# Kernel optimization log

Hardware: AMD Instinct MI355X
Metric: run time of the kernel (lower is better)

Reference implementation:

```python
import jax, jax.numpy as jnp
import numpy as np

BIT = 8          # mantissa bits (incl. sign) shared-exponent BFP
GROUP_SIZE = 16  # elements sharing one exponent


def bfp_quant(x, bit=BIT, group_size=GROUP_SIZE):
    """Block floating-point quantization: flatten, group, share max exponent per group."""
    orig_shape = x.shape
    flat = x.reshape(-1)
    n = flat.shape[0]
    pad = (-n) % group_size
    flat = jnp.pad(flat, (0, pad))
    g = flat.reshape(-1, group_size)                      # [G, group_size]
    m = jnp.max(jnp.abs(g), axis=1, keepdims=True)        # shared magnitude per group
    e = jnp.floor(jnp.log2(jnp.where(m > 0, m, 1.0)))     # shared exponent
    scale = jnp.exp2(e - (bit - 1))                       # quantization step
    qmax = 2.0 ** (bit - 1) - 1
    q = jnp.clip(jnp.round(g / scale), -qmax, qmax) * scale
    q = jnp.where(m > 0, q, 0.0)                          # all-zero groups stay zero
    return q.reshape(-1)[:n].reshape(orig_shape)


def conv2d(x, w, stride=1, padding=1):
    return jax.lax.conv_general_dilated(
        x, w,
        window_strides=(stride, stride),
        padding=((padding, padding), (padding, padding)),
        dimension_numbers=("NCHW", "OIHW", "NCHW"),
    )


def setup_inputs() -> dict:
    key = jax.random.key(0)
    k1, k2 = jax.random.split(key)
    x = jax.random.normal(k1, (64, 128, 56, 56), dtype=jnp.float32)
    fan_in = 128 * 3 * 3
    bound = 1.0 / np.sqrt(fan_in)  # kaiming_uniform_(a=sqrt(5)) -> U(-1/sqrt(fan_in), 1/sqrt(fan_in))
    w = jax.random.uniform(k2, (128, 128, 3, 3), dtype=jnp.float32,
                           minval=-bound, maxval=bound)
    return {"x": x, "w": w}


def reference(x, w):
    # BFConv2dFunction.forward: quantize both operands then conv2d (bias=None, stride=1, padding=1)
    return conv2d(bfp_quant(x), bfp_quant(w), stride=1, padding=1)
```

## Files before the change

kernel.cpp:

```cpp
#include <hip/hip_runtime.h>
#include <hip/hip_bf16.h>


using short8 = __attribute__((ext_vector_type(8))) short;
using f32x4  = __attribute__((ext_vector_type(4))) float;
using int4v  = __attribute__((ext_vector_type(4))) int;

#define XS_STRIDE_S 40
#define XS_ENT      348
#define XS_BUF_S    (XS_ENT * XS_STRIDE_S)

__device__ __forceinline__ unsigned short f2bf(float f) {
    union { float f; unsigned u; } v; v.f = f;
    return (unsigned short)(v.u >> 16);
}

__device__ __forceinline__ void quant16(const float* v, float* o) {
    float m = 0.f;
    #pragma unroll
    for (int i = 0; i < 16; ++i) m = fmaxf(m, fabsf(v[i]));
    if (m > 0.f) {
        float e     = floorf(log2f(m));
        float scale = exp2f(e - 7.0f);
        float inv   = exp2f(7.0f - e);
        #pragma unroll
        for (int i = 0; i < 16; ++i) {
            float q = rintf(v[i] * inv);
            q = fminf(fmaxf(q, -127.f), 127.f);
            o[i] = q * scale;
        }
    } else {
        #pragma unroll
        for (int i = 0; i < 16; ++i) o[i] = 0.f;
    }
}

__global__ __launch_bounds__(256) void quant_x_kernel(const float* __restrict__ x,
                                                      unsigned short* __restrict__ xq) {
    const int bid = blockIdx.x;
    const int n  = bid / 98;
    const int pb = bid % 98;
    const int t  = threadIdx.x;
    const int c  = t & 127;
    const int g  = t >> 7;
    const int p0 = pb * 32 + g * 16;

    const float* src = x + ((size_t)(n * 128 + c) * 3136 + p0);
    float v[16];
    #pragma unroll
    for (int i = 0; i < 4; ++i) {
        float4 f = *reinterpret_cast<const float4*>(src + i * 4);
        v[i*4+0] = f.x; v[i*4+1] = f.y; v[i*4+2] = f.z; v[i*4+3] = f.w;
    }
    float o[16];
    quant16(v, o);
    unsigned short* dst = xq + ((size_t)(n * 3136 + p0) * 128 + c);
    #pragma unroll
    for (int j = 0; j < 16; ++j) dst[(size_t)j * 128] = f2bf(o[j]);
}

__global__ __launch_bounds__(256) void quant_w_kernel(const float* __restrict__ w,
                                                      unsigned short* __restrict__ wq) {
    const int G = blockIdx.x * 256 + threadIdx.x;
    const int k    = G / 72;
    const int base = (G % 72) * 16;
    const float* src = w + (size_t)k * 1152 + base;
    float v[16];
    #pragma unroll
    for (int i = 0; i < 4; ++i) {
        float4 f = *reinterpret_cast<const float4*>(src + i * 4);
        v[i*4+0] = f.x; v[i*4+1] = f.y; v[i*4+2] = f.z; v[i*4+3] = f.w;
    }
    float o[16];
    quant16(v, o);
    #pragma unroll
    for (int j = 0; j < 16; ++j) {
        int idx2 = base + j;
        int c  = idx2 / 9;
        int rs = idx2 % 9;
        wq[(((size_t)(c >> 5) * 9 + rs) * 128 + k) * 32 + (c & 31)] = f2bf(o[j]);
    }
}

__global__ __launch_bounds__(256, 2) void conv_kernel(const unsigned short* __restrict__ xq,
                                                      const unsigned short* __restrict__ wq,
                                                      float* __restrict__ out) {
    __shared__ __align__(16) unsigned short Xs[2 * XS_BUF_S];

    const int bid  = blockIdx.x;
    const int n    = bid / 14;
    const int h0   = (bid % 14) * 4;
    const int t    = threadIdx.x;
    const int lane = t & 63;
    const int wave = t >> 6;
    const int mw   = wave >> 1;
    const int nw   = wave & 1;

    const unsigned short* sbase[6];
    int  soff[6];
    bool svalid[6], sact[6];
    #pragma unroll
    for (int it = 0; it < 6; ++it) {
        int i   = t + it * 256;
        bool act = i < 1392;
        int e   = i >> 2, cc = i & 3;
        int row = e / 58, pw = e % 58;
        int h   = h0 - 1 + row, w_ = pw - 1;
        bool inb = act && (unsigned)h < 56u && (unsigned)w_ < 56u;
        int gidx = inb ? (n * 3136 + h * 56 + w_) : 0;
        sbase[it]  = xq + (size_t)gidx * 128 + cc * 8;
        soff[it]   = e * XS_STRIDE_S + cc * 8;
        svalid[it] = inb;
        sact[it]   = act;
    }
    int4v sreg[6];

#define STAGE_LOAD(CB) do {                                                    \
    _Pragma("unroll")                                                          \
    for (int it = 0; it < 6; ++it)                                             \
        sreg[it] = svalid[it]                                                  \
            ? *reinterpret_cast<const int4v*>(sbase[it] + (CB) * 32)           \
            : int4v{0, 0, 0, 0};                                               \
} while (0)

#define STAGE_WRITE(BUFS) do {                                                 \
    _Pragma("unroll")                                                          \
    for (int it = 0; it < 6; ++it)                                             \
        if (sact[it])                                                          \
            *reinterpret_cast<int4v*>(Xs + (BUFS) + soff[it]) = sreg[it];      \
} while (0)

    int boff[7];
    #pragma unroll
    for (int fi = 0; fi < 7; ++fi) {
        int m  = mw * 112 + fi * 16 + (lane & 15);
        int dh = m / 56, w_ = m % 56;
        boff[fi] = (dh * 58 + w_) * XS_STRIDE_S + ((lane >> 4) * 8);
    }
    const unsigned short* wk = wq + (size_t)(nw * 64 + (lane & 15)) * 32 + ((lane >> 4) * 8);

    f32x4 acc[7][4];
    #pragma unroll
    for (int fi = 0; fi < 7; ++fi)
        #pragma unroll
        for (int ni = 0; ni < 4; ++ni)
            acc[fi][ni] = f32x4{0.f, 0.f, 0.f, 0.f};

#define RS_STEP(RS) do {                                                       \
    const int rsS = (((RS) / 3) * 58 + ((RS) % 3)) * XS_STRIDE_S;              \
    short8 a[4], b[7];                                                         \
    _Pragma("unroll")                                                          \
    for (int ni = 0; ni < 4; ++ni)                                             \
        a[ni] = *reinterpret_cast<const short8*>(wcb + (RS) * 4096 + ni * 512);\
    _Pragma("unroll")                                                          \
    for (int fi = 0; fi < 7; ++fi)                                             \
        b[fi] = *reinterpret_cast<const short8*>(Xs + bufS + boff[fi] + rsS);  \
    _Pragma("unroll")                                                          \
    for (int fi = 0; fi < 7; ++fi)                                             \
        _Pragma("unroll")                                                      \
        for (int ni = 0; ni < 4; ++ni)                                         \
            acc[fi][ni] = __builtin_amdgcn_mfma_f32_16x16x32_bf16(             \
                a[ni], b[fi], acc[fi][ni], 0, 0, 0);                           \
} while (0)

    STAGE_LOAD(0);
    STAGE_WRITE(0);
    __syncthreads();

    for (int cblk = 0; cblk < 4; ++cblk) {
        const int bufS = (cblk & 1) * XS_BUF_S;
        const unsigned short* wcb = wk + (size_t)cblk * 9 * 4096;
        RS_STEP(0);
        if (cblk < 3) STAGE_LOAD(cblk + 1);
        RS_STEP(1); RS_STEP(2); RS_STEP(3); RS_STEP(4);
        RS_STEP(5); RS_STEP(6); RS_STEP(7); RS_STEP(8);
        if (cblk < 3) STAGE_WRITE(((cblk + 1) & 1) * XS_BUF_S);
        __syncthreads();
    }

    const int pix0  = h0 * 56 + mw * 112 + (lane & 15);
    const int krow0 = n * 128 + nw * 64 + ((lane >> 4) * 4);
    #pragma unroll
    for (int fi = 0; fi < 7; ++fi)
        #pragma unroll
        for (int ni = 0; ni < 4; ++ni)
            #pragma unroll
            for (int j = 0; j < 4; ++j)
                out[(size_t)(krow0 + ni * 16 + j) * 3136 + pix0 + fi * 16] = acc[fi][ni][j];
#undef RS_STEP
#undef STAGE_LOAD
#undef STAGE_WRITE
}

extern "C" void kernel_launch(void* const* d_in, const int* in_sizes, int n_in,
                              void* d_out, int out_size, void* d_ws, size_t ws_size,
                              hipStream_t stream) {
    const float* x = (const float*)d_in[0];
    const float* w = (const float*)d_in[1];
    float* out = (float*)d_out;

    unsigned short* xq = (unsigned short*)d_ws;
    unsigned short* wq = xq + (size_t)25690112;

    quant_x_kernel<<<64 * 98, 256, 0, stream>>>(x, xq);
    quant_w_kernel<<<36,      256, 0, stream>>>(w, wq);
    conv_kernel  <<<896,      256, 0, stream>>>(xq, wq, out);
}
```

Measured before the change: 272.9 us.

## Merge quant kernels with LDS transpose, swizzle conv blocks, prefetch weight fragments

Folds the x and w quantization into one launch, and stages each 128-channel by 64-pixel tile of x through shared memory so global reads are coalesced before the per-channel group quantization. The conv kernel remaps block indices so consecutive blocks come from different images, and it fully unrolls the 36 channel-block/tap steps with a one-step-ahead register prefetch of the weight fragments. This aims to cut launch overhead and uncoalesced-access cost and to hide global weight-load latency behind the MFMAs. In exchange it uses more registers, which could hurt occupancy under the two-blocks-per-CU bound.

```diff
diff --git a/kernel.cpp b/kernel.cpp
--- a/kernel.cpp
+++ b/kernel.cpp
@@ -35,50 +35,64 @@
     }
 }
 
-__global__ __launch_bounds__(256) void quant_x_kernel(const float* __restrict__ x,
-                                                      unsigned short* __restrict__ xq) {
+__global__ __launch_bounds__(256) void quant_kernel(const float* __restrict__ x,
+                                                    const float* __restrict__ w,
+                                                    unsigned short* __restrict__ xq,
+                                                    unsigned short* __restrict__ wq) {
+    __shared__ float T[128 * 68];
     const int bid = blockIdx.x;
-    const int n  = bid / 98;
-    const int pb = bid % 98;
-    const int t  = threadIdx.x;
-    const int c  = t & 127;
-    const int g  = t >> 7;
-    const int p0 = pb * 32 + g * 16;
-
-    const float* src = x + ((size_t)(n * 128 + c) * 3136 + p0);
-    float v[16];
-    #pragma unroll
-    for (int i = 0; i < 4; ++i) {
-        float4 f = *reinterpret_cast<const float4*>(src + i * 4);
-        v[i*4+0] = f.x; v[i*4+1] = f.y; v[i*4+2] = f.z; v[i*4+3] = f.w;
-    }
-    float o[16];
-    quant16(v, o);
-    unsigned short* dst = xq + ((size_t)(n * 3136 + p0) * 128 + c);
-    #pragma unroll
-    for (int j = 0; j < 16; ++j) dst[(size_t)j * 128] = f2bf(o[j]);
-}
-
-__global__ __launch_bounds__(256) void quant_w_kernel(const float* __restrict__ w,
-                                                      unsigned short* __restrict__ wq) {
-    const int G = blockIdx.x * 256 + threadIdx.x;
-    const int k    = G / 72;
-    const int base = (G % 72) * 16;
-    const float* src = w + (size_t)k * 1152 + base;
-    float v[16];
-    #pragma unroll
-    for (int i = 0; i < 4; ++i) {
-        float4 f = *reinterpret_cast<const float4*>(src + i * 4);
-        v[i*4+0] = f.x; v[i*4+1] = f.y; v[i*4+2] = f.z; v[i*4+3] = f.w;
-    }
-    float o[16];
-    quant16(v, o);
-    #pragma unroll
-    for (int j = 0; j < 16; ++j) {
-        int idx2 = base + j;
-        int c  = idx2 / 9;
-        int rs = idx2 % 9;
-        wq[(((size_t)(c >> 5) * 9 + rs) * 128 + k) * 32 + (c & 31)] = f2bf(o[j]);
+    const int t   = threadIdx.x;
+
+    if (bid < 3136) {
+        const int n  = bid / 49;
+        const int p0 = (bid % 49) * 64;
+        const float* src = x + (size_t)n * 128 * 3136 + p0;
+
+        #pragma unroll
+        for (int i = 0; i < 8; ++i) {
+            const int c  = (t >> 4) + i * 16;
+            const int ch = t & 15;
+            *reinterpret_cast<float4*>(&T[c * 68 + ch * 4]) =
+                *reinterpret_cast<const float4*>(src + (size_t)c * 3136 + ch * 4);
+        }
+        __syncthreads();
+
+        const int c = t & 127;
+        #pragma unroll
+        for (int i = 0; i < 2; ++i) {
+            const int grp = (t >> 7) + 2 * i;
+            float v[16];
+            #pragma unroll
+            for (int j2 = 0; j2 < 4; ++j2) {
+                float4 f = *reinterpret_cast<const float4*>(&T[c * 68 + grp * 16 + j2 * 4]);
+                v[j2*4+0] = f.x; v[j2*4+1] = f.y; v[j2*4+2] = f.z; v[j2*4+3] = f.w;
+            }
+            float o[16];
+            quant16(v, o);
+            unsigned short* dst = xq + ((size_t)(n * 3136 + p0 + grp * 16)) * 128 + c;
+            #pragma unroll
+            for (int j = 0; j < 16; ++j) dst[(size_t)j * 128] = f2bf(o[j]);
+        }
+    } else {
+        const int G    = (bid - 3136) * 256 + t;
+        const int k    = G / 72;
+        const int base = (G % 72) * 16;
+        const float* src = w + (size_t)k * 1152 + base;
+        float v[16];
+        #pragma unroll
+        for (int i = 0; i < 4; ++i) {
+            float4 f = *reinterpret_cast<const float4*>(src + i * 4);
+            v[i*4+0] = f.x; v[i*4+1] = f.y; v[i*4+2] = f.z; v[i*4+3] = f.w;
+        }
+        float o[16];
+        quant16(v, o);
+        #pragma unroll
+        for (int j = 0; j < 16; ++j) {
+            int idx2 = base + j;
+            int c  = idx2 / 9;
+            int rs = idx2 % 9;
+            wq[(((size_t)(c >> 5) * 9 + rs) * 128 + k) * 32 + (c & 31)] = f2bf(o[j]);
+        }
     }
 }
 
@@ -87,7 +101,8 @@
                                                       float* __restrict__ out) {
     __shared__ __align__(16) unsigned short Xs[2 * XS_BUF_S];
 
-    const int bid  = blockIdx.x;
+    const int b0   = blockIdx.x;
+    const int bid  = (b0 & 7) * 112 + (b0 >> 3);
     const int n    = bid / 14;
     const int h0   = (bid % 14) * 4;
     const int t    = threadIdx.x;
@@ -139,6 +154,13 @@
     }
     const unsigned short* wk = wq + (size_t)(nw * 64 + (lane & 15)) * 32 + ((lane >> 4) * 8);
 
+#define LOADA(DST, STEP) do {                                                  \
+    _Pragma("unroll")                                                          \
+    for (int ni = 0; ni < 4; ++ni)                                             \
+        DST[ni] = *reinterpret_cast<const short8*>(                            \
+            wk + (size_t)(STEP) * 4096 + ni * 512);                            \
+} while (0)
+
     f32x4 acc[7][4];
     #pragma unroll
     for (int fi = 0; fi < 7; ++fi)
@@ -146,36 +168,41 @@
         for (int ni = 0; ni < 4; ++ni)
             acc[fi][ni] = f32x4{0.f, 0.f, 0.f, 0.f};
 
-#define RS_STEP(RS) do {                                                       \
-    const int rsS = (((RS) / 3) * 58 + ((RS) % 3)) * XS_STRIDE_S;              \
-    short8 a[4], b[7];                                                         \
-    _Pragma("unroll")                                                          \
-    for (int ni = 0; ni < 4; ++ni)                                             \
-        a[ni] = *reinterpret_cast<const short8*>(wcb + (RS) * 4096 + ni * 512);\
-    _Pragma("unroll")                                                          \
-    for (int fi = 0; fi < 7; ++fi)                                             \
-        b[fi] = *reinterpret_cast<const short8*>(Xs + bufS + boff[fi] + rsS);  \
-    _Pragma("unroll")                                                          \
-    for (int fi = 0; fi < 7; ++fi)                                             \
-        _Pragma("unroll")                                                      \
-        for (int ni = 0; ni < 4; ++ni)                                         \
-            acc[fi][ni] = __builtin_amdgcn_mfma_f32_16x16x32_bf16(             \
-                a[ni], b[fi], acc[fi][ni], 0, 0, 0);                           \
-} while (0)
+    short8 a_cur[4], a_nxt[4];
 
     STAGE_LOAD(0);
+    LOADA(a_cur, 0);
     STAGE_WRITE(0);
     __syncthreads();
 
-    for (int cblk = 0; cblk < 4; ++cblk) {
+    #pragma unroll
+    for (int step = 0; step < 36; ++step) {
+        const int cblk = step / 9;
+        const int rs   = step % 9;
         const int bufS = (cblk & 1) * XS_BUF_S;
-        const unsigned short* wcb = wk + (size_t)cblk * 9 * 4096;
-        RS_STEP(0);
-        if (cblk < 3) STAGE_LOAD(cblk + 1);
-        RS_STEP(1); RS_STEP(2); RS_STEP(3); RS_STEP(4);
-        RS_STEP(5); RS_STEP(6); RS_STEP(7); RS_STEP(8);
-        if (cblk < 3) STAGE_WRITE(((cblk + 1) & 1) * XS_BUF_S);
-        __syncthreads();
+
+        if (step < 35) LOADA(a_nxt, step + 1);
+        if (rs == 0 && cblk < 3) STAGE_LOAD(cblk + 1);
+
+        const int rsS = ((rs / 3) * 58 + (rs % 3)) * XS_STRIDE_S;
+        short8 b[7];
+        #pragma unroll
+        for (int fi = 0; fi < 7; ++fi)
+            b[fi] = *reinterpret_cast<const short8*>(Xs + bufS + boff[fi] + rsS);
+
+        #pragma unroll
+        for (int fi = 0; fi < 7; ++fi)
+            #pragma unroll
+            for (int ni = 0; ni < 4; ++ni)
+                acc[fi][ni] = __builtin_amdgcn_mfma_f32_16x16x32_bf16(
+                    a_cur[ni], b[fi], acc[fi][ni], 0, 0, 0);
+
+        if (rs == 8) {
+            if (cblk < 3) STAGE_WRITE(((cblk + 1) & 1) * XS_BUF_S);
+            __syncthreads();
+        }
+        #pragma unroll
+        for (int ni = 0; ni < 4; ++ni) a_cur[ni] = a_nxt[ni];
     }
 
     const int pix0  = h0 * 56 + mw * 112 + (lane & 15);
@@ -187,7 +214,7 @@
             #pragma unroll
             for (int j = 0; j < 4; ++j)
                 out[(size_t)(krow0 + ni * 16 + j) * 3136 + pix0 + fi * 16] = acc[fi][ni][j];
-#undef RS_STEP
+#undef LOADA
 #undef STAGE_LOAD
 #undef STAGE_WRITE
 }
@@ -202,7 +229,6 @@
     unsigned short* xq = (unsigned short*)d_ws;
     unsigned short* wq = xq + (size_t)25690112;
 
-    quant_x_kernel<<<64 * 98, 256, 0, stream>>>(x, xq);
-    quant_w_kernel<<<36,      256, 0, stream>>>(w, wq);
-    conv_kernel  <<<896,      256, 0, stream>>>(xq, wq, out);
-}
+    quant_kernel<<<3136 + 36, 256, 0, stream>>>(x, w, xq, wq);
+    conv_kernel <<<896,       256, 0, stream>>>(xq, wq, out);
+}
```

New measurement: 257.5 us. 5.7% less time.
